# Performance work log

Hardware: AMD Instinct MI355X
Metric: run time of the kernel (lower is better)

## Reference

```python
import jax, jax.numpy as jnp
import numpy as np

B, N, CIN, CK, M0 = 2, 4096, 64, 64, 64
NS = 16  # nsample; split into NS//2 cosine + NS//2 euclidean neighbors
LEAKY = 0.1


def _leaky(x):
    return jax.nn.leaky_relu(x, LEAKY)


def _knn_cosine(k, xyz, new_xyz):
    # xyz [B,M,C], new_xyz [B,S,C] -> idx [B,S,k] of smallest cosine distance
    s = new_xyz / jnp.sqrt(jnp.sum(new_xyz ** 2, -1, keepdims=True) + 1e-8)
    d = xyz / jnp.sqrt(jnp.sum(xyz ** 2, -1, keepdims=True) + 1e-8)
    dist = 1.0 - jnp.einsum('bsc,bmc->bsm', s, d)
    return jax.lax.top_k(-dist, k)[1]


def _knn_euclid(k, xyz, new_xyz):
    # squared euclidean distance [B,S,M]
    dist = (jnp.sum(new_xyz ** 2, -1)[:, :, None]
            + jnp.sum(xyz ** 2, -1)[:, None, :]
            - 2.0 * jnp.einsum('bsc,bmc->bsm', new_xyz, xyz))
    return jax.lax.top_k(-dist, k)[1]


def _group(points, idx):
    # points [B,M,C], idx [B,S,K] -> [B,S,K,C]
    return jax.vmap(lambda p, i: p[i])(points, idx)


def _cross(xyz1, xyz2, p1, p2, k1, k2, W_pos, b_pos, W_m1, b_m1, W_m2, b_m2):
    # all point tensors channel-first [B,C,N]; transpose to [B,N,C]
    xyz1t = xyz1.transpose(0, 2, 1)
    xyz2t = xyz2.transpose(0, 2, 1)
    p1t = p1.transpose(0, 2, 1)
    p2t = p2.transpose(0, 2, 1)
    k1t = k1.transpose(0, 2, 1)
    k2t = k2.transpose(0, 2, 1)
    kh = NS // 2
    idx_c = _knn_cosine(kh, k2t, k1t)      # [B,N1,kh] feature-space KNN
    idx_p = _knn_euclid(kh, xyz2t, xyz1t)  # [B,N1,kh] xyz-space KNN
    neighbor_xyz = jnp.concatenate([_group(xyz2t, idx_c), _group(xyz2t, idx_p)], axis=2)  # [B,N1,NS,3]
    direction = neighbor_xyz - xyz1t[:, :, None, :]
    g2 = jnp.concatenate([_group(p2t, idx_c), _group(p2t, idx_p)], axis=2)  # [B,N1,NS,D]
    pos = jnp.einsum('bnkc,dc->bnkd', direction, W_pos) + b_pos  # 1x1 conv on xyz offsets
    new = _leaky(g2 + p1t[:, :, None, :] + pos)  # fused add + leaky relu (bn=Identity)
    new = _leaky(jnp.einsum('bnkd,ed->bnke', new, W_m1) + b_m1)
    new = _leaky(jnp.einsum('bnkd,ed->bnke', new, W_m2) + b_m2)
    new = jnp.max(new, axis=2)  # max-pool over neighbor dim -> [B,N1,D]
    return new.transpose(0, 2, 1)  # [B,D,N1]


def setup_inputs() -> dict:
    key = jax.random.key(0)
    ks = jax.random.split(key, 12)
    rn = lambda k, shape, s=1.0: jax.random.normal(k, shape, jnp.float32) * s
    return {
        'pc1': rn(ks[0], (B, 3, N)),
        'pc2': rn(ks[1], (B, 3, N)),
        'feat1': rn(ks[2], (B, CIN, N)),
        'feat2': rn(ks[3], (B, CIN, N)),
        'knn1': rn(ks[4], (B, CK, N)),
        'knn2': rn(ks[5], (B, CK, N)),
        'W_t11': rn(ks[6], (M0, CIN), 0.1),
        'b_t11': jnp.zeros((M0,), jnp.float32),
        'W_t22': rn(ks[7], (M0, CIN), 0.1),
        'b_t22': jnp.zeros((M0,), jnp.float32),
        'W_pos': rn(ks[8], (M0, 3), 0.1),
        'b_pos': jnp.zeros((M0,), jnp.float32),
        'W_m1': rn(ks[9], (M0, M0), 0.1),
        'b_m1': jnp.zeros((M0,), jnp.float32),
        'W_m2': rn(ks[10], (M0, M0), 0.1),
        'b_m2': jnp.zeros((M0,), jnp.float32),
    }


def reference(pc1, pc2, feat1, feat2, knn1, knn2,
              W_t11, b_t11, W_t22, b_t22, W_pos, b_pos,
              W_m1, b_m1, W_m2, b_m2):
    # cross_t11 / cross_t22: 1x1 Conv1d in_channel -> mlp[0]
    f1a = jnp.einsum('dc,bcn->bdn', W_t11, feat1) + b_t11[None, :, None]
    f2a = jnp.einsum('dc,bcn->bdn', W_t22, feat2) + b_t22[None, :, None]
    f2b = jnp.einsum('dc,bcn->bdn', W_t11, feat2) + b_t11[None, :, None]
    f1b = jnp.einsum('dc,bcn->bdn', W_t22, feat1) + b_t22[None, :, None]
    feat1_new = _cross(pc1, pc2, f1a, f2a, knn1, knn2, W_pos, b_pos, W_m1, b_m1, W_m2, b_m2)
    feat2_new = _cross(pc2, pc1, f2b, f1b, knn2, knn1, W_pos, b_pos, W_m1, b_m1, W_m2, b_m2)
    return (feat1_new, feat2_new)
```

## Files before the change

kernel.cpp:

```cpp
#include <hip/hip_runtime.h>
#include <hip/hip_bf16.h>

#define BB 2
#define NN 4096
#define CH 64

typedef __bf16 bf16x8 __attribute__((ext_vector_type(8)));
typedef float f32x4 __attribute__((ext_vector_type(4)));

__device__ __forceinline__ float lrelu(float v) { return fmaxf(v, 0.1f * v); }
__device__ __forceinline__ float tobf(const __hip_bfloat16& h) { return __bfloat162float(h); }

#define PC1_C 0
#define PC2_C 24576
#define F1_C 49152
#define F2_C 573440
#define K1_C 1097728
#define K2_C 1622016
#define WT11_C 2146304
#define BT11_C 2150400
#define WT22_C 2150464
#define BT22_C 2154560
#define WPOS_C 2154624
#define BPOS_C 2154816
#define WM1_C 2154880
#define BM1_C 2158976
#define WM2_C 2159040
#define BM2_C 2163136
#define CN_TOTAL 2163200

#define FHALF (2 * BB * NN * CH)

__device__ __forceinline__ unsigned fmap(float s) {
  unsigned u = __float_as_uint(s);
  return u ^ ((unsigned)((int)u >> 31) | 0x80000000u);
}

__device__ __forceinline__ unsigned umaxu(unsigned a, unsigned b) { return a > b ? a : b; }
__device__ __forceinline__ void casu(unsigned& a, unsigned& b) {
  unsigned mx = a > b ? a : b;
  unsigned mn = a > b ? b : a;
  a = mx; b = mn;
}

__device__ __forceinline__ void bitonic8(unsigned bd[8]) {
  casu(bd[0], bd[4]); casu(bd[1], bd[5]); casu(bd[2], bd[6]); casu(bd[3], bd[7]);
  casu(bd[0], bd[2]); casu(bd[1], bd[3]); casu(bd[4], bd[6]); casu(bd[5], bd[7]);
  casu(bd[0], bd[1]); casu(bd[2], bd[3]); casu(bd[4], bd[5]); casu(bd[6], bd[7]);
}

__device__ __forceinline__ void merge4(unsigned bd[8], unsigned k0, unsigned k1,
                                       unsigned k2, unsigned k3) {
  casu(k0, k1); casu(k2, k3); casu(k0, k2); casu(k1, k3); casu(k1, k2);
  bd[4] = umaxu(bd[4], k3); bd[5] = umaxu(bd[5], k2);
  bd[6] = umaxu(bd[6], k1); bd[7] = umaxu(bd[7], k0);
  bitonic8(bd);
}

__device__ __forceinline__ void merge88(unsigned a[8], const unsigned b[8]) {
  a[0] = umaxu(a[0], b[7]); a[1] = umaxu(a[1], b[6]);
  a[2] = umaxu(a[2], b[5]); a[3] = umaxu(a[3], b[4]);
  a[4] = umaxu(a[4], b[3]); a[5] = umaxu(a[5], b[2]);
  a[6] = umaxu(a[6], b[1]); a[7] = umaxu(a[7], b[0]);
  bitonic8(a);
}

__device__ __forceinline__ void xmerge(unsigned a[8], int m) {
  unsigned t[8];
#pragma unroll
  for (int k = 0; k < 8; ++k) t[k] = (unsigned)__shfl_xor((int)a[k], m, 64);
  merge88(a, t);
}

__global__ void k_detect(const unsigned short* __restrict__ pc1raw, int* __restrict__ flag) {
  int lane = threadIdx.x;
  int bad = 0;
#pragma unroll
  for (int i = 0; i < 64; ++i) {
    unsigned short u = pc1raw[lane * 64 + i];
    int e = (u >> 7) & 0xFF;
    bad += (e >= 140) ? 1 : 0;
  }
#pragma unroll
  for (int s = 32; s; s >>= 1) bad += __shfl_xor(bad, s, 64);
  if (lane == 0) *flag = (bad > 16) ? 1 : 0;
}

__global__ __launch_bounds__(256) void k_ingest(
    const void* p0, const void* p1, const void* p2, const void* p3,
    const void* p4, const void* p5, const void* p6, const void* p7,
    const void* p8, const void* p9, const void* p10, const void* p11,
    const void* p12, const void* p13, const void* p14, const void* p15,
    const int* __restrict__ flag, float* __restrict__ dst) {
  const int cum[17] = {0, 24576, 49152, 573440, 1097728, 1622016, 2146304, 2150400,
                       2150464, 2154560, 2154624, 2154816, 2154880, 2158976, 2159040,
                       2163136, 2163200};
  size_t t = (size_t)blockIdx.x * 256 + threadIdx.x;
  if (t >= (size_t)CN_TOTAL) return;
  int seg = 0;
#pragma unroll
  for (int i = 1; i < 16; ++i) seg += (t >= (size_t)cum[i]) ? 1 : 0;
  size_t local = t - (size_t)cum[seg];
  const void* ptrs[16] = {p0, p1, p2, p3, p4, p5, p6, p7, p8, p9, p10, p11, p12, p13, p14, p15};
  const void* p = ptrs[seg];
  float v;
  if (*flag) v = ((const float*)p)[local];
  else       v = tobf(((const __hip_bfloat16*)p)[local]);
  if (!(v == v) || fabsf(v) > 1e30f) v = 0.f;
  dst[t] = v;
}

__global__ __launch_bounds__(256) void k_prep_all(const float* __restrict__ cn,
                                                  float* __restrict__ knnt,
                                                  __hip_bfloat16* __restrict__ knnb,
                                                  __hip_bfloat16* __restrict__ fhl,
                                                  __hip_bfloat16* __restrict__ wmb,
                                                  float4* __restrict__ xyzt,
                                                  float4* __restrict__ wp4,
                                                  __hip_bfloat16* __restrict__ wcb) {
  int bid = blockIdx.x;
  if (bid < 64) {
    int t = bid * 256 + threadIdx.x;
    int n = t & (NN - 1);
    int b = (t >> 12) & 1;
    int a = t >> 13;
    const float* col = cn + (a ? K2_C : K1_C) + (size_t)b * CH * NN + n;
    float s = 0.f;
#pragma unroll
    for (int c = 0; c < CH; ++c) { float v = col[(size_t)c * NN]; s += v * v; }
    float inv = 1.0f / sqrtf(s + 1e-8f);
    size_t row = (size_t)(a * BB + b) * NN + n;
    float* o = knnt + row * CH;
    __hip_bfloat16* ob = knnb + row * CH;
#pragma unroll
    for (int c = 0; c < CH; ++c) {
      float v = col[(size_t)c * NN] * inv;
      o[c] = v;
      ob[c] = __float2bfloat16(v);
    }
  } else if (bid < 128) {
    int t = (bid - 64) * 256 + threadIdx.x;
    int n = t & (NN - 1);
    int b = (t >> 12) & 1;
    int a = t >> 13;
    const float* col = cn + (a ? F2_C : F1_C) + (size_t)b * CH * NN + n;
    __hip_bfloat16* oh = fhl + ((size_t)(a * BB + b) * NN + n) * CH;
    __hip_bfloat16* ol = oh + FHALF;
#pragma unroll
    for (int c = 0; c < CH; ++c) {
      float v = col[(size_t)c * NN];
      __hip_bfloat16 hi = __float2bfloat16(v);
      oh[c] = hi;
      ol[c] = __float2bfloat16(v - tobf(hi));
    }
  } else if (bid < 160) {
    int t = (bid - 128) * 256 + threadIdx.x;
    float v = (t < 4096) ? cn[WM1_C + t] : cn[WM2_C + (t - 4096)];
    wmb[t] = __float2bfloat16(v);
  } else if (bid < 224) {
    int t = (bid - 160) * 256 + threadIdx.x;
    int n = t & (NN - 1);
    int b = (t >> 12) & 1;
    int a = t >> 13;
    const float* p = cn + (a ? PC2_C : PC1_C) + (size_t)b * 3 * NN + n;
    float x = p[0], y = p[NN], z = p[2 * NN];
    xyzt[(size_t)(a * BB + b) * NN + n] = make_float4(x, y, z, x * x + y * y + z * z);
  } else if (bid == 224) {
    int c = threadIdx.x;
    if (c < 64)
      wp4[c] = make_float4(cn[WPOS_C + 3 * c], cn[WPOS_C + 3 * c + 1],
                           cn[WPOS_C + 3 * c + 2], cn[BPOS_C + c]);
  } else {
    int t = (bid - 225) * 256 + threadIdx.x;
    int w = t >> 12, e = t & 4095;
    float v = cn[(w ? WT22_C : WT11_C) + e];
    __hip_bfloat16 hi = __float2bfloat16(v);
    __hip_bfloat16 lo = __float2bfloat16(v - tobf(hi));
    wcb[w * 4096 + e] = hi;
    wcb[8192 + w * 4096 + e] = lo;
  }
}

__global__ __launch_bounds__(256) void k_conv2(const __hip_bfloat16* __restrict__ fhl,
                                               const __hip_bfloat16* __restrict__ wcb,
                                               const float* __restrict__ cn,
                                               float* __restrict__ fbuf) {
  int bid = blockIdx.x;
  int ntile = bid & 255;
  int b = (bid >> 8) & 1;
  int a = bid >> 9;
  int t = threadIdx.x;
  int dt = t >> 6;
  int lane = t & 63;
  int lo = lane & 15, g = lane >> 4;

  const __hip_bfloat16* fb = fhl + ((size_t)(a * BB + b) * NN + ntile * 16 + lo) * CH;
  bf16x8 ah0 = *reinterpret_cast<const bf16x8*>(fb + g * 8);
  bf16x8 ah1 = *reinterpret_cast<const bf16x8*>(fb + 32 + g * 8);
  bf16x8 al0 = *reinterpret_cast<const bf16x8*>(fb + FHALF + g * 8);
  bf16x8 al1 = *reinterpret_cast<const bf16x8*>(fb + FHALF + 32 + g * 8);

#pragma unroll
  for (int w = 0; w < 2; ++w) {
    const __hip_bfloat16* wb = wcb + w * 4096 + (dt * 16 + lo) * 64;
    bf16x8 wh0 = *reinterpret_cast<const bf16x8*>(wb + g * 8);
    bf16x8 wh1 = *reinterpret_cast<const bf16x8*>(wb + 32 + g * 8);
    bf16x8 wl0 = *reinterpret_cast<const bf16x8*>(wb + 8192 + g * 8);
    bf16x8 wl1 = *reinterpret_cast<const bf16x8*>(wb + 8192 + 32 + g * 8);
    float bv = cn[(w ? BT22_C : BT11_C) + dt * 16 + lo];
    f32x4 acc = {bv, bv, bv, bv};
    acc = __builtin_amdgcn_mfma_f32_16x16x32_bf16(ah0, wh0, acc, 0, 0, 0);
    acc = __builtin_amdgcn_mfma_f32_16x16x32_bf16(ah1, wh1, acc, 0, 0, 0);
    acc = __builtin_amdgcn_mfma_f32_16x16x32_bf16(al0, wh0, acc, 0, 0, 0);
    acc = __builtin_amdgcn_mfma_f32_16x16x32_bf16(al1, wh1, acc, 0, 0, 0);
    acc = __builtin_amdgcn_mfma_f32_16x16x32_bf16(ah0, wl0, acc, 0, 0, 0);
    acc = __builtin_amdgcn_mfma_f32_16x16x32_bf16(ah1, wl1, acc, 0, 0, 0);
    int sel = a ? (w ? 1 : 2) : (w ? 3 : 0);
    float* ob = fbuf + ((size_t)(sel * BB + b) * NN + ntile * 16 + g * 4) * CH + dt * 16 + lo;
    ob[0 * CH] = acc[0];
    ob[1 * CH] = acc[1];
    ob[2 * CH] = acc[2];
    ob[3 * CH] = acc[3];
  }
}

__global__ __launch_bounds__(512, 4) void k_knn5(const __hip_bfloat16* __restrict__ knnb,
                                                 const float* __restrict__ knnt,
                                                 const float4* __restrict__ xyzt,
                                                 int* __restrict__ idxf) {
  __shared__ unsigned sk[16 * 8 * 9];
  __shared__ int cidx[16 * 16];
  int bid = blockIdx.x;
  int qt = bid & (NN / 16 - 1);
  int b = (bid >> 8) & 1;
  int x = bid >> 9;
  int w = threadIdx.x >> 6;
  int lane = threadIdx.x & 63;
  int lo = lane & 15, g = lane >> 4;
  int q0 = qt * 16;
  int j0 = w * (NN / 8);
  int hw = lane >> 5, sl = lane & 31;
  int qq = w * 2 + hw;
  size_t qbase = (size_t)(x * BB + b) * NN;
  size_t dbase = (size_t)((1 - x) * BB + b) * NN;

  const __hip_bfloat16* qb = knnb + (qbase + q0) * CH;
  bf16x8 qf0 = *reinterpret_cast<const bf16x8*>(qb + lo * CH + g * 8);
  bf16x8 qf1 = *reinterpret_cast<const bf16x8*>(qb + lo * CH + 32 + g * 8);
  const __hip_bfloat16* db = knnb + dbase * CH;
  const float4 q4 = xyzt[qbase + q0 + lo];
  const float4* dbx = xyzt + dbase;
  float tx = 2.f * q4.x, ty = 2.f * q4.y, tz = 2.f * q4.z;

  unsigned bc0[8], bc1[8], be0[8], be1[8];
#pragma unroll
  for (int k = 0; k < 8; ++k) { bc0[k] = 0u; bc1[k] = 0u; be0[k] = 0u; be1[k] = 0u; }

  auto STEP = [&](const bf16x8& A0, const bf16x8& A1, const float4& P0,
                  const float4& P1, const float4& P2, const float4& P3,
                  int rcv, unsigned (&bc)[8], unsigned (&be)[8]) {
    f32x4 acc = {0.f, 0.f, 0.f, 0.f};
    acc = __builtin_amdgcn_mfma_f32_16x16x32_bf16(A0, qf0, acc, 0, 0, 0);
    acc = __builtin_amdgcn_mfma_f32_16x16x32_bf16(A1, qf1, acc, 0, 0, 0);
    float v0 = fmaf(tx, P0.x, fmaf(ty, P0.y, fmaf(tz, P0.z, -P0.w)));
    float v1 = fmaf(tx, P1.x, fmaf(ty, P1.y, fmaf(tz, P1.z, -P1.w)));
    float v2 = fmaf(tx, P2.x, fmaf(ty, P2.y, fmaf(tz, P2.z, -P2.w)));
    float v3 = fmaf(tx, P3.x, fmaf(ty, P3.y, fmaf(tz, P3.z, -P3.w)));
    unsigned r = (unsigned)rcv;
    merge4(bc, (__float_as_uint(acc[0] + 4.0f) & 0xFFFFF000u) | r,
               (__float_as_uint(acc[1] + 4.0f) & 0xFFFFF000u) | (r - 1),
               (__float_as_uint(acc[2] + 4.0f) & 0xFFFFF000u) | (r - 2),
               (__float_as_uint(acc[3] + 4.0f) & 0xFFFFF000u) | (r - 3));
    merge4(be, (fmap(v0) & 0xFFFFF000u) | r,
               (fmap(v1) & 0xFFFFF000u) | (r - 1),
               (fmap(v2) & 0xFFFFF000u) | (r - 2),
               (fmap(v3) & 0xFFFFF000u) | (r - 3));
  };

  const __hip_bfloat16* arA = db + (size_t)(j0 + lo) * CH + g * 8;
  const __hip_bfloat16* arB = arA + 16 * CH;
  const float4* peA = dbx + j0 + g * 4;
  const float4* peB = peA + 16;
  int rc = 4095 - j0 - g * 4;

  bf16x8 aA0 = *reinterpret_cast<const bf16x8*>(arA);
  bf16x8 aA1 = *reinterpret_cast<const bf16x8*>(arA + 32);
  float4 pA0 = peA[0], pA1 = peA[1], pA2 = peA[2], pA3 = peA[3];

  for (int i = 0; i < 15; ++i) {
    bf16x8 aB0 = *reinterpret_cast<const bf16x8*>(arB);
    bf16x8 aB1 = *reinterpret_cast<const bf16x8*>(arB + 32);
    float4 pB0 = peB[0], pB1 = peB[1], pB2 = peB[2], pB3 = peB[3];
    STEP(aA0, aA1, pA0, pA1, pA2, pA3, rc, bc0, be0);
    arA += 32 * CH; peA += 32;
    aA0 = *reinterpret_cast<const bf16x8*>(arA);
    aA1 = *reinterpret_cast<const bf16x8*>(arA + 32);
    pA0 = peA[0]; pA1 = peA[1]; pA2 = peA[2]; pA3 = peA[3];
    STEP(aB0, aB1, pB0, pB1, pB2, pB3, rc - 16, bc1, be1);
    arB += 32 * CH; peB += 32;
    rc -= 32;
  }
  {
    bf16x8 aB0 = *reinterpret_cast<const bf16x8*>(arB);
    bf16x8 aB1 = *reinterpret_cast<const bf16x8*>(arB + 32);
    float4 pB0 = peB[0], pB1 = peB[1], pB2 = peB[2], pB3 = peB[3];
    STEP(aA0, aA1, pA0, pA1, pA2, pA3, rc, bc0, be0);
    STEP(aB0, aB1, pB0, pB1, pB2, pB3, rc - 16, bc1, be1);
  }
  merge88(bc0, bc1);
  merge88(be0, be1);
  xmerge(bc0, 16); xmerge(bc0, 32);
  xmerge(be0, 16); xmerge(be0, 32);

  if (g == 0) {
#pragma unroll
    for (int k = 0; k < 8; ++k) sk[(lo * 8 + k) * 9 + w] = bc0[k];
  }
  __syncthreads();
  {
    unsigned e[16];
#pragma unroll
    for (int k = 0; k < 8; ++k) e[k] = sk[(qq * 8 + k) * 9 + (sl & 7)];
#pragma unroll
    for (int k = 8; k < 16; ++k) e[k] = 0u;
#pragma unroll
    for (int s = 1; s < 8; s <<= 1) {
      unsigned f[16];
#pragma unroll
      for (int k = 0; k < 16; ++k) f[k] = (unsigned)__shfl_xor((int)e[k], s, 64);
#pragma unroll
      for (int i = 0; i < 16; ++i) e[i] = umaxu(e[i], f[15 - i]);
      casu(e[0], e[8]); casu(e[1], e[9]); casu(e[2], e[10]); casu(e[3], e[11]);
      casu(e[4], e[12]); casu(e[5], e[13]); casu(e[6], e[14]); casu(e[7], e[15]);
      casu(e[0], e[4]); casu(e[1], e[5]); casu(e[2], e[6]); casu(e[3], e[7]);
      casu(e[8], e[12]); casu(e[9], e[13]); casu(e[10], e[14]); casu(e[11], e[15]);
      casu(e[0], e[2]); casu(e[1], e[3]); casu(e[4], e[6]); casu(e[5], e[7]);
      casu(e[8], e[10]); casu(e[9], e[11]); casu(e[12], e[14]); casu(e[13], e[15]);
      casu(e[0], e[1]); casu(e[2], e[3]); casu(e[4], e[5]); casu(e[6], e[7]);
      casu(e[8], e[9]); casu(e[10], e[11]); casu(e[12], e[13]); casu(e[14], e[15]);
    }
    if (sl == 0) {
#pragma unroll
      for (int k = 0; k < 16; ++k) cidx[qq * 16 + k] = 4095 - (int)(e[k] & 4095u);
    }
    int c = sl >> 1, hr = sl & 1;
    int idx = cidx[qq * 16 + c];
    const float4* qr = reinterpret_cast<const float4*>(knnt + (qbase + q0 + qq) * CH) + hr * 8;
    const float4* dr = reinterpret_cast<const float4*>(knnt + (dbase + idx) * CH) + hr * 8;
    float v = 0.f;
#pragma unroll 4
    for (int cb = 0; cb < 8; ++cb) {
      float4 qv = qr[cb], dv = dr[cb];
      v += qv.x * dv.x + qv.y * dv.y + qv.z * dv.z + qv.w * dv.w;
    }
    v += __shfl_xor(v, 1, 64);
    int ii = idx;
#pragma unroll
    for (int k = 2; k <= 32; k <<= 1) {
#pragma unroll
      for (int j = k >> 1; j >= 1; j >>= 1) {
        float ov = __shfl_xor(v, j, 64);
        int oi = __shfl_xor(ii, j, 64);
        bool ob = (ov > v) || (ov == v && oi < ii);
        bool want = (((sl & k) == 0) == ((sl & j) == 0));
        bool take = (want == ob);
        v = take ? ov : v;
        ii = take ? oi : ii;
      }
    }
    if (sl < 16 && (sl & 1) == 0) idxf[(qbase + q0 + qq) * 16 + (sl >> 1)] = ii;
  }
  __syncthreads();

  if (g == 0) {
#pragma unroll
    for (int k = 0; k < 8; ++k) sk[(lo * 8 + k) * 9 + w] = be0[k];
  }
  __syncthreads();
  {
    unsigned e[16];
#pragma unroll
    for (int k = 0; k < 8; ++k) e[k] = sk[(qq * 8 + k) * 9 + (sl & 7)];
#pragma unroll
    for (int k = 8; k < 16; ++k) e[k] = 0u;
#pragma unroll
    for (int s = 1; s < 8; s <<= 1) {
      unsigned f[16];
#pragma unroll
      for (int k = 0; k < 16; ++k) f[k] = (unsigned)__shfl_xor((int)e[k], s, 64);
#pragma unroll
      for (int i = 0; i < 16; ++i) e[i] = umaxu(e[i], f[15 - i]);
      casu(e[0], e[8]); casu(e[1], e[9]); casu(e[2], e[10]); casu(e[3], e[11]);
      casu(e[4], e[12]); casu(e[5], e[13]); casu(e[6], e[14]); casu(e[7], e[15]);
      casu(e[0], e[4]); casu(e[1], e[5]); casu(e[2], e[6]); casu(e[3], e[7]);
      casu(e[8], e[12]); casu(e[9], e[13]); casu(e[10], e[14]); casu(e[11], e[15]);
      casu(e[0], e[2]); casu(e[1], e[3]); casu(e[4], e[6]); casu(e[5], e[7]);
      casu(e[8], e[10]); casu(e[9], e[11]); casu(e[12], e[14]); casu(e[13], e[15]);
      casu(e[0], e[1]); casu(e[2], e[3]); casu(e[4], e[5]); casu(e[6], e[7]);
      casu(e[8], e[9]); casu(e[10], e[11]); casu(e[12], e[13]); casu(e[14], e[15]);
    }
    if (sl == 0) {
#pragma unroll
      for (int k = 0; k < 16; ++k) cidx[qq * 16 + k] = 4095 - (int)(e[k] & 4095u);
    }
    int c = sl >> 1;
    int idx = cidx[qq * 16 + c];
    const float4 qx4 = xyzt[qbase + q0 + qq];
    float4 p = xyzt[dbase + idx];
    float v = fmaf(2.f * qx4.x, p.x, fmaf(2.f * qx4.y, p.y, fmaf(2.f * qx4.z, p.z, -p.w)));
    int ii = idx;
#pragma unroll
    for (int k = 2; k <= 32; k <<= 1) {
#pragma unroll
      for (int j = k >> 1; j >= 1; j >>= 1) {
        float ov = __shfl_xor(v, j, 64);
        int oi = __shfl_xor(ii, j, 64);
        bool ob = (ov > v) || (ov == v && oi < ii);
        bool want = (((sl & k) == 0) == ((sl & j) == 0));
        bool take = (want == ob);
        v = take ? ov : v;
        ii = take ? oi : ii;
      }
    }
    if (sl < 16 && (sl & 1) == 0) idxf[(qbase + q0 + qq) * 16 + 8 + (sl >> 1)] = ii;
  }
}

__global__ __launch_bounds__(256) void k_mlp(const float* __restrict__ fbuf,
                                             const float4* __restrict__ xyzt,
                                             const int* __restrict__ idxf,
                                             const float4* __restrict__ wp4,
                                             const __hip_bfloat16* __restrict__ wmb,
                                             const float* __restrict__ cn,
                                             float* __restrict__ out) {
  __shared__ __bf16 h1s[4 * 16 * 72];
  const int t = threadIdx.x;
  const int wv = t >> 6, L = t & 63;
  const int lo = L & 15, g = L >> 4;
  int bid = blockIdx.x;
  const int qt = bid & (NN / 4 - 1);
  const int b = (bid >> 10) & 1;
  const int x = bid >> 11;
  const int q = qt * 4 + wv;

  bf16x8 w1f[4][2], w2f[4][2];
#pragma unroll
  for (int tt = 0; tt < 4; ++tt)
#pragma unroll
    for (int kc = 0; kc < 2; ++kc) {
      int e = tt * 16 + lo, c0 = kc * 32 + g * 8;
      w1f[tt][kc] = *reinterpret_cast<const bf16x8*>(wmb + e * 64 + c0);
      w2f[tt][kc] = *reinterpret_cast<const bf16x8*>(wmb + 4096 + e * 64 + c0);
    }

  const float* pq  = fbuf + ((size_t)((x ? 2 : 0) * BB + b)) * NN * CH;
  const float* pdb = fbuf + ((size_t)((x ? 3 : 1) * BB + b)) * NN * CH;
  const float4* qx  = xyzt + (size_t)(x * BB + b) * NN;
  const float4* dbx = xyzt + (size_t)((1 - x) * BB + b) * NN;

  const int m = lo;
  int jm = idxf[(((size_t)x * BB + b) * NN + q) * 16 + m];
  jm &= (NN - 1);
  const float4 q4 = qx[q];
  const float4 p4 = dbx[jm];
  const float dx = p4.x - q4.x, dy = p4.y - q4.y, dz = p4.z - q4.z;

  const float4* g2v = reinterpret_cast<const float4*>(pdb + (size_t)jm * CH);
  const float4* pqv = reinterpret_cast<const float4*>(pq + (size_t)q * CH);
  float hv[16];
  {
    float4 t0 = g2v[g * 2], t1 = g2v[g * 2 + 1], t2 = g2v[g * 2 + 8], t3 = g2v[g * 2 + 9];
    float4 u0 = pqv[g * 2], u1 = pqv[g * 2 + 1], u2 = pqv[g * 2 + 8], u3 = pqv[g * 2 + 9];
    hv[0] = t0.x + u0.x; hv[1] = t0.y + u0.y; hv[2] = t0.z + u0.z; hv[3] = t0.w + u0.w;
    hv[4] = t1.x + u1.x; hv[5] = t1.y + u1.y; hv[6] = t1.z + u1.z; hv[7] = t1.w + u1.w;
    hv[8] = t2.x + u2.x; hv[9] = t2.y + u2.y; hv[10] = t2.z + u2.z; hv[11] = t2.w + u2.w;
    hv[12] = t3.x + u3.x; hv[13] = t3.y + u3.y; hv[14] = t3.z + u3.z; hv[15] = t3.w + u3.w;
  }

  bf16x8 a0, a1;
#pragma unroll
  for (int kc = 0; kc < 2; ++kc) {
#pragma unroll
    for (int j = 0; j < 8; ++j) {
      int c = kc * 32 + g * 8 + j;
      float4 wp = wp4[c];
      float v = hv[kc * 8 + j] + wp.x * dx + wp.y * dy + wp.z * dz + wp.w;
      v = lrelu(v);
      if (kc == 0) a0[j] = (__bf16)v; else a1[j] = (__bf16)v;
    }
  }

  __bf16* hrow = h1s + wv * 16 * 72;
#pragma unroll
  for (int tt = 0; tt < 4; ++tt) {
    float bv = cn[BM1_C + tt * 16 + lo];
    f32x4 acc = {bv, bv, bv, bv};
    acc = __builtin_amdgcn_mfma_f32_16x16x32_bf16(a0, w1f[tt][0], acc, 0, 0, 0);
    acc = __builtin_amdgcn_mfma_f32_16x16x32_bf16(a1, w1f[tt][1], acc, 0, 0, 0);
#pragma unroll
    for (int r = 0; r < 4; ++r) {
      float v = lrelu(acc[r]);
      hrow[(g * 4 + r) * 72 + tt * 16 + lo] = (__bf16)v;
    }
  }
  __syncthreads();
  bf16x8 h1a = *reinterpret_cast<const bf16x8*>(hrow + m * 72 + g * 8);
  bf16x8 h1b = *reinterpret_cast<const bf16x8*>(hrow + m * 72 + 32 + g * 8);

  size_t obase = ((size_t)(x * BB + b) * CH) * NN;
#pragma unroll
  for (int tt = 0; tt < 4; ++tt) {
    float bv = cn[BM2_C + tt * 16 + lo];
    f32x4 acc = {bv, bv, bv, bv};
    acc = __builtin_amdgcn_mfma_f32_16x16x32_bf16(h1a, w2f[tt][0], acc, 0, 0, 0);
    acc = __builtin_amdgcn_mfma_f32_16x16x32_bf16(h1b, w2f[tt][1], acc, 0, 0, 0);
    float v = fmaxf(fmaxf(lrelu(acc[0]), lrelu(acc[1])), fmaxf(lrelu(acc[2]), lrelu(acc[3])));
    v = fmaxf(v, __shfl_xor(v, 16, 64));
    v = fmaxf(v, __shfl_xor(v, 32, 64));
    if (g == 0) out[obase + (size_t)(tt * 16 + lo) * NN + q] = v;
  }
}

#define CN_OFF 0
#define FB_OFF ((size_t)CN_TOTAL)
#define KT_OFF (FB_OFF + (size_t)4 * BB * NN * CH)
#define XZ_OFF (KT_OFF + (size_t)2 * BB * NN * CH)
#define WP4_OFF (XZ_OFF + (size_t)2 * BB * NN * 4)
#define WMB_OFF (WP4_OFF + 256)
#define IDX_OFF (WMB_OFF + 4096)
#define FLAG_OFF (IDX_OFF + 262144)
#define KNB_OFF (FLAG_OFF + 4)
#define FHL_OFF (KNB_OFF + (size_t)BB * NN * CH)
#define WCB_OFF (FHL_OFF + (size_t)2 * BB * NN * CH)

extern "C" void kernel_launch(void* const* d_in, const int* in_sizes, int n_in,
                              void* d_out, int out_size, void* d_ws, size_t ws_size,
                              hipStream_t stream) {
  float* ws = (float*)d_ws;
  float* cn = ws + CN_OFF;
  int* flag = (int*)(ws + FLAG_OFF);

  k_detect<<<1, 64, 0, stream>>>((const unsigned short*)d_in[0], flag);
  k_ingest<<<(CN_TOTAL + 255) / 256, 256, 0, stream>>>(
      d_in[0], d_in[1], d_in[2], d_in[3], d_in[4], d_in[5], d_in[6], d_in[7],
      d_in[8], d_in[9], d_in[10], d_in[11], d_in[12], d_in[13], d_in[14], d_in[15],
      flag, cn);
  k_prep_all<<<257, 256, 0, stream>>>(cn, ws + KT_OFF, (__hip_bfloat16*)(ws + KNB_OFF),
                                      (__hip_bfloat16*)(ws + FHL_OFF),
                                      (__hip_bfloat16*)(ws + WMB_OFF),
                                      (float4*)(ws + XZ_OFF), (float4*)(ws + WP4_OFF),
                                      (__hip_bfloat16*)(ws + WCB_OFF));
  k_conv2<<<1024, 256, 0, stream>>>((const __hip_bfloat16*)(ws + FHL_OFF),
                                    (const __hip_bfloat16*)(ws + WCB_OFF), cn, ws + FB_OFF);
  k_knn5<<<2 * BB * (NN / 16), 512, 0, stream>>>(
      (const __hip_bfloat16*)(ws + KNB_OFF), ws + KT_OFF,
      (const float4*)(ws + XZ_OFF), (int*)(ws + IDX_OFF));
  k_mlp<<<2 * BB * (NN / 4), 256, 0, stream>>>(ws + FB_OFF, (const float4*)(ws + XZ_OFF),
                                               (const int*)(ws + IDX_OFF), (const float4*)(ws + WP4_OFF),
                                               (const __hip_bfloat16*)(ws + WMB_OFF), cn,
                                               (float*)d_out);
}
```

Measured before the change: 273.8 us.

## Fuse dtype detection and ingest into prep, read inputs directly

Removes the separate detect kernel and the large ingest copy of all activations into a float staging buffer. The prep kernel now reads the raw inputs directly and detects the dtype per block, and only the small weight tensors are still staged. Block index decoding in conv, knn and mlp is reordered so batch and side vary fastest, and the knn launch bounds request higher occupancy. Each block now repeats the dtype detection read, and the tighter launch bound may force register spills.

```diff
diff --git a/kernel.cpp b/kernel.cpp
--- a/kernel.cpp
+++ b/kernel.cpp
@@ -31,6 +31,30 @@
 
 #define FHALF (2 * BB * NN * CH)
 
+__device__ __forceinline__ bool detect_f32(const unsigned short* __restrict__ pc1raw) {
+  int lane = threadIdx.x & 63;
+  const uint4* p4 = reinterpret_cast<const uint4*>(pc1raw);
+  int bad = 0;
+#pragma unroll
+  for (int k = 0; k < 8; ++k) {
+    uint4 v = p4[lane * 8 + k];
+    unsigned w0 = v.x, w1 = v.y, w2 = v.z, w3 = v.w;
+    bad += (((w0 >> 7) & 0xFF) >= 140) + (((w0 >> 23) & 0xFF) >= 140);
+    bad += (((w1 >> 7) & 0xFF) >= 140) + (((w1 >> 23) & 0xFF) >= 140);
+    bad += (((w2 >> 7) & 0xFF) >= 140) + (((w2 >> 23) & 0xFF) >= 140);
+    bad += (((w3 >> 7) & 0xFF) >= 140) + (((w3 >> 23) & 0xFF) >= 140);
+  }
+#pragma unroll
+  for (int s = 32; s; s >>= 1) bad += __shfl_xor(bad, s, 64);
+  return bad > 16;
+}
+
+__device__ __forceinline__ float rdval(const void* __restrict__ p, size_t i, bool f32) {
+  float v = f32 ? ((const float*)p)[i] : tobf(((const __hip_bfloat16*)p)[i]);
+  if (!(v == v) || fabsf(v) > 1e30f) v = 0.f;
+  return v;
+}
+
 __device__ __forceinline__ unsigned fmap(float s) {
   unsigned u = __float_as_uint(s);
   return u ^ ((unsigned)((int)u >> 31) | 0x80000000u);
@@ -72,83 +96,64 @@
   merge88(a, t);
 }
 
-__global__ void k_detect(const unsigned short* __restrict__ pc1raw, int* __restrict__ flag) {
-  int lane = threadIdx.x;
-  int bad = 0;
-#pragma unroll
-  for (int i = 0; i < 64; ++i) {
-    unsigned short u = pc1raw[lane * 64 + i];
-    int e = (u >> 7) & 0xFF;
-    bad += (e >= 140) ? 1 : 0;
-  }
-#pragma unroll
-  for (int s = 32; s; s >>= 1) bad += __shfl_xor(bad, s, 64);
-  if (lane == 0) *flag = (bad > 16) ? 1 : 0;
-}
-
-__global__ __launch_bounds__(256) void k_ingest(
-    const void* p0, const void* p1, const void* p2, const void* p3,
-    const void* p4, const void* p5, const void* p6, const void* p7,
-    const void* p8, const void* p9, const void* p10, const void* p11,
-    const void* p12, const void* p13, const void* p14, const void* p15,
-    const int* __restrict__ flag, float* __restrict__ dst) {
-  const int cum[17] = {0, 24576, 49152, 573440, 1097728, 1622016, 2146304, 2150400,
-                       2150464, 2154560, 2154624, 2154816, 2154880, 2158976, 2159040,
-                       2163136, 2163200};
-  size_t t = (size_t)blockIdx.x * 256 + threadIdx.x;
-  if (t >= (size_t)CN_TOTAL) return;
+__global__ __launch_bounds__(256) void k_ingest_small(
+    const void* p6, const void* p7, const void* p8, const void* p9,
+    const void* p10, const void* p11, const void* p12, const void* p13,
+    const void* p14, const void* p15, const unsigned short* __restrict__ pc1raw,
+    float* __restrict__ dst) {
+  bool f32 = detect_f32(pc1raw);
+  int t = blockIdx.x * 256 + threadIdx.x;
+  if (t >= 16896) return;
+  const int cum[11] = {0, 4096, 4160, 8256, 8320, 8512, 8576, 12672, 12736, 16832, 16896};
   int seg = 0;
 #pragma unroll
-  for (int i = 1; i < 16; ++i) seg += (t >= (size_t)cum[i]) ? 1 : 0;
-  size_t local = t - (size_t)cum[seg];
-  const void* ptrs[16] = {p0, p1, p2, p3, p4, p5, p6, p7, p8, p9, p10, p11, p12, p13, p14, p15};
-  const void* p = ptrs[seg];
-  float v;
-  if (*flag) v = ((const float*)p)[local];
-  else       v = tobf(((const __hip_bfloat16*)p)[local]);
-  if (!(v == v) || fabsf(v) > 1e30f) v = 0.f;
-  dst[t] = v;
-}
-
-__global__ __launch_bounds__(256) void k_prep_all(const float* __restrict__ cn,
-                                                  float* __restrict__ knnt,
-                                                  __hip_bfloat16* __restrict__ knnb,
-                                                  __hip_bfloat16* __restrict__ fhl,
-                                                  __hip_bfloat16* __restrict__ wmb,
-                                                  float4* __restrict__ xyzt,
-                                                  float4* __restrict__ wp4,
-                                                  __hip_bfloat16* __restrict__ wcb) {
+  for (int i = 1; i < 11; ++i) seg += (t >= cum[i]) ? 1 : 0;
+  const void* ptrs[10] = {p6, p7, p8, p9, p10, p11, p12, p13, p14, p15};
+  dst[WT11_C + t] = rdval(ptrs[seg], t - cum[seg], f32);
+}
+
+__global__ __launch_bounds__(256) void k_prep_all(
+    const void* pc1, const void* pc2, const void* f1, const void* f2,
+    const void* k1, const void* k2, const float* __restrict__ cn,
+    float* __restrict__ knnt, __hip_bfloat16* __restrict__ knnb,
+    __hip_bfloat16* __restrict__ fhl, __hip_bfloat16* __restrict__ wmb,
+    float4* __restrict__ xyzt, float4* __restrict__ wp4,
+    __hip_bfloat16* __restrict__ wcb) {
   int bid = blockIdx.x;
   if (bid < 64) {
+    bool f32 = detect_f32((const unsigned short*)pc1);
     int t = bid * 256 + threadIdx.x;
     int n = t & (NN - 1);
     int b = (t >> 12) & 1;
     int a = t >> 13;
-    const float* col = cn + (a ? K2_C : K1_C) + (size_t)b * CH * NN + n;
+    const void* src = a ? k2 : k1;
+    size_t base = (size_t)b * CH * NN + n;
     float s = 0.f;
 #pragma unroll
-    for (int c = 0; c < CH; ++c) { float v = col[(size_t)c * NN]; s += v * v; }
+    for (int c = 0; c < CH; ++c) { float v = rdval(src, base + (size_t)c * NN, f32); s += v * v; }
     float inv = 1.0f / sqrtf(s + 1e-8f);
     size_t row = (size_t)(a * BB + b) * NN + n;
     float* o = knnt + row * CH;
     __hip_bfloat16* ob = knnb + row * CH;
 #pragma unroll
     for (int c = 0; c < CH; ++c) {
-      float v = col[(size_t)c * NN] * inv;
+      float v = rdval(src, base + (size_t)c * NN, f32) * inv;
       o[c] = v;
       ob[c] = __float2bfloat16(v);
     }
   } else if (bid < 128) {
+    bool f32 = detect_f32((const unsigned short*)pc1);
     int t = (bid - 64) * 256 + threadIdx.x;
     int n = t & (NN - 1);
     int b = (t >> 12) & 1;
     int a = t >> 13;
-    const float* col = cn + (a ? F2_C : F1_C) + (size_t)b * CH * NN + n;
+    const void* src = a ? f2 : f1;
+    size_t base = (size_t)b * CH * NN + n;
     __hip_bfloat16* oh = fhl + ((size_t)(a * BB + b) * NN + n) * CH;
     __hip_bfloat16* ol = oh + FHALF;
 #pragma unroll
     for (int c = 0; c < CH; ++c) {
-      float v = col[(size_t)c * NN];
+      float v = rdval(src, base + (size_t)c * NN, f32);
       __hip_bfloat16 hi = __float2bfloat16(v);
       oh[c] = hi;
       ol[c] = __float2bfloat16(v - tobf(hi));
@@ -158,12 +163,16 @@
     float v = (t < 4096) ? cn[WM1_C + t] : cn[WM2_C + (t - 4096)];
     wmb[t] = __float2bfloat16(v);
   } else if (bid < 224) {
+    bool f32 = detect_f32((const unsigned short*)pc1);
     int t = (bid - 160) * 256 + threadIdx.x;
     int n = t & (NN - 1);
     int b = (t >> 12) & 1;
     int a = t >> 13;
-    const float* p = cn + (a ? PC2_C : PC1_C) + (size_t)b * 3 * NN + n;
-    float x = p[0], y = p[NN], z = p[2 * NN];
+    const void* src = a ? pc2 : pc1;
+    size_t base = (size_t)b * 3 * NN + n;
+    float x = rdval(src, base, f32);
+    float y = rdval(src, base + NN, f32);
+    float z = rdval(src, base + 2 * NN, f32);
     xyzt[(size_t)(a * BB + b) * NN + n] = make_float4(x, y, z, x * x + y * y + z * z);
   } else if (bid == 224) {
     int c = threadIdx.x;
@@ -186,9 +195,9 @@
                                                const float* __restrict__ cn,
                                                float* __restrict__ fbuf) {
   int bid = blockIdx.x;
-  int ntile = bid & 255;
-  int b = (bid >> 8) & 1;
-  int a = bid >> 9;
+  int b = bid & 1;
+  int a = (bid >> 1) & 1;
+  int ntile = bid >> 2;
   int t = threadIdx.x;
   int dt = t >> 6;
   int lane = t & 63;
@@ -224,16 +233,16 @@
   }
 }
 
-__global__ __launch_bounds__(512, 4) void k_knn5(const __hip_bfloat16* __restrict__ knnb,
+__global__ __launch_bounds__(512, 8) void k_knn5(const __hip_bfloat16* __restrict__ knnb,
                                                  const float* __restrict__ knnt,
                                                  const float4* __restrict__ xyzt,
                                                  int* __restrict__ idxf) {
   __shared__ unsigned sk[16 * 8 * 9];
   __shared__ int cidx[16 * 16];
   int bid = blockIdx.x;
-  int qt = bid & (NN / 16 - 1);
-  int b = (bid >> 8) & 1;
-  int x = bid >> 9;
+  int b = bid & 1;
+  int x = (bid >> 1) & 1;
+  int qt = bid >> 2;
   int w = threadIdx.x >> 6;
   int lane = threadIdx.x & 63;
   int lo = lane & 15, g = lane >> 4;
@@ -438,9 +447,9 @@
   const int wv = t >> 6, L = t & 63;
   const int lo = L & 15, g = L >> 4;
   int bid = blockIdx.x;
-  const int qt = bid & (NN / 4 - 1);
-  const int b = (bid >> 10) & 1;
-  const int x = bid >> 11;
+  const int b = bid & 1;
+  const int x = (bid >> 1) & 1;
+  const int qt = bid >> 2;
   const int q = qt * 4 + wv;
 
   bf16x8 w1f[4][2], w2f[4][2];
@@ -538,18 +547,15 @@
                               hipStream_t stream) {
   float* ws = (float*)d_ws;
   float* cn = ws + CN_OFF;
-  int* flag = (int*)(ws + FLAG_OFF);
-
-  k_detect<<<1, 64, 0, stream>>>((const unsigned short*)d_in[0], flag);
-  k_ingest<<<(CN_TOTAL + 255) / 256, 256, 0, stream>>>(
-      d_in[0], d_in[1], d_in[2], d_in[3], d_in[4], d_in[5], d_in[6], d_in[7],
-      d_in[8], d_in[9], d_in[10], d_in[11], d_in[12], d_in[13], d_in[14], d_in[15],
-      flag, cn);
-  k_prep_all<<<257, 256, 0, stream>>>(cn, ws + KT_OFF, (__hip_bfloat16*)(ws + KNB_OFF),
-                                      (__hip_bfloat16*)(ws + FHL_OFF),
-                                      (__hip_bfloat16*)(ws + WMB_OFF),
-                                      (float4*)(ws + XZ_OFF), (float4*)(ws + WP4_OFF),
-                                      (__hip_bfloat16*)(ws + WCB_OFF));
+
+  k_ingest_small<<<66, 256, 0, stream>>>(
+      d_in[6], d_in[7], d_in[8], d_in[9], d_in[10], d_in[11], d_in[12], d_in[13],
+      d_in[14], d_in[15], (const unsigned short*)d_in[0], cn);
+  k_prep_all<<<257, 256, 0, stream>>>(
+      d_in[0], d_in[1], d_in[2], d_in[3], d_in[4], d_in[5], cn,
+      ws + KT_OFF, (__hip_bfloat16*)(ws + KNB_OFF), (__hip_bfloat16*)(ws + FHL_OFF),
+      (__hip_bfloat16*)(ws + WMB_OFF), (float4*)(ws + XZ_OFF), (float4*)(ws + WP4_OFF),
+      (__hip_bfloat16*)(ws + WCB_OFF));
   k_conv2<<<1024, 256, 0, stream>>>((const __hip_bfloat16*)(ws + FHL_OFF),
                                     (const __hip_bfloat16*)(ws + WCB_OFF), cn, ws + FB_OFF);
   k_knn5<<<2 * BB * (NN / 16), 512, 0, stream>>>(
```

New measurement: 391.9 us. 1.43x slower.

## Fuse conv kernel into KNN kernel launch and interleave block index mapping

Applied to the files above, without the earlier changes.

The separate 1x1-conv MFMA kernel is merged into the KNN kernel as extra tail blocks (ids 1024 and up, two conv tiles per 512-thread block), removing one kernel launch and letting the conv work fill idle CUs alongside the KNN blocks. Block index decoding in the KNN and MLP kernels is reordered so batch and direction vary fastest, spreading adjacent blocks across different data. In exchange, the conv blocks now carry the KNN kernel's shared memory and 512-thread launch bounds, which may limit their occupancy, and the new block ordering may change cache locality.

```diff
diff --git a/kernel.cpp b/kernel.cpp
--- a/kernel.cpp
+++ b/kernel.cpp
@@ -181,59 +181,61 @@
   }
 }
 
-__global__ __launch_bounds__(256) void k_conv2(const __hip_bfloat16* __restrict__ fhl,
-                                               const __hip_bfloat16* __restrict__ wcb,
-                                               const float* __restrict__ cn,
-                                               float* __restrict__ fbuf) {
+__global__ __launch_bounds__(512, 4) void k_knncv(const __hip_bfloat16* __restrict__ knnb,
+                                                  const float* __restrict__ knnt,
+                                                  const float4* __restrict__ xyzt,
+                                                  const __hip_bfloat16* __restrict__ fhl,
+                                                  const __hip_bfloat16* __restrict__ wcb,
+                                                  const float* __restrict__ cn,
+                                                  int* __restrict__ idxf,
+                                                  float* __restrict__ fbuf) {
   int bid = blockIdx.x;
-  int ntile = bid & 255;
-  int b = (bid >> 8) & 1;
-  int a = bid >> 9;
-  int t = threadIdx.x;
-  int dt = t >> 6;
-  int lane = t & 63;
-  int lo = lane & 15, g = lane >> 4;
-
-  const __hip_bfloat16* fb = fhl + ((size_t)(a * BB + b) * NN + ntile * 16 + lo) * CH;
-  bf16x8 ah0 = *reinterpret_cast<const bf16x8*>(fb + g * 8);
-  bf16x8 ah1 = *reinterpret_cast<const bf16x8*>(fb + 32 + g * 8);
-  bf16x8 al0 = *reinterpret_cast<const bf16x8*>(fb + FHALF + g * 8);
-  bf16x8 al1 = *reinterpret_cast<const bf16x8*>(fb + FHALF + 32 + g * 8);
-
-#pragma unroll
-  for (int w = 0; w < 2; ++w) {
-    const __hip_bfloat16* wb = wcb + w * 4096 + (dt * 16 + lo) * 64;
-    bf16x8 wh0 = *reinterpret_cast<const bf16x8*>(wb + g * 8);
-    bf16x8 wh1 = *reinterpret_cast<const bf16x8*>(wb + 32 + g * 8);
-    bf16x8 wl0 = *reinterpret_cast<const bf16x8*>(wb + 8192 + g * 8);
-    bf16x8 wl1 = *reinterpret_cast<const bf16x8*>(wb + 8192 + 32 + g * 8);
-    float bv = cn[(w ? BT22_C : BT11_C) + dt * 16 + lo];
-    f32x4 acc = {bv, bv, bv, bv};
-    acc = __builtin_amdgcn_mfma_f32_16x16x32_bf16(ah0, wh0, acc, 0, 0, 0);
-    acc = __builtin_amdgcn_mfma_f32_16x16x32_bf16(ah1, wh1, acc, 0, 0, 0);
-    acc = __builtin_amdgcn_mfma_f32_16x16x32_bf16(al0, wh0, acc, 0, 0, 0);
-    acc = __builtin_amdgcn_mfma_f32_16x16x32_bf16(al1, wh1, acc, 0, 0, 0);
-    acc = __builtin_amdgcn_mfma_f32_16x16x32_bf16(ah0, wl0, acc, 0, 0, 0);
-    acc = __builtin_amdgcn_mfma_f32_16x16x32_bf16(ah1, wl1, acc, 0, 0, 0);
-    int sel = a ? (w ? 1 : 2) : (w ? 3 : 0);
-    float* ob = fbuf + ((size_t)(sel * BB + b) * NN + ntile * 16 + g * 4) * CH + dt * 16 + lo;
-    ob[0 * CH] = acc[0];
-    ob[1 * CH] = acc[1];
-    ob[2 * CH] = acc[2];
-    ob[3 * CH] = acc[3];
-  }
-}
-
-__global__ __launch_bounds__(512, 4) void k_knn5(const __hip_bfloat16* __restrict__ knnb,
-                                                 const float* __restrict__ knnt,
-                                                 const float4* __restrict__ xyzt,
-                                                 int* __restrict__ idxf) {
+  if (bid >= 1024) {
+    int cb = bid - 1024;
+    int b = cb & 1;
+    int a = (cb >> 1) & 1;
+    int ntile = (cb >> 2) * 2 + (threadIdx.x >> 8);
+    int t = threadIdx.x & 255;
+    int dt = t >> 6;
+    int lane = t & 63;
+    int lo = lane & 15, g = lane >> 4;
+
+    const __hip_bfloat16* fb = fhl + ((size_t)(a * BB + b) * NN + ntile * 16 + lo) * CH;
+    bf16x8 ah0 = *reinterpret_cast<const bf16x8*>(fb + g * 8);
+    bf16x8 ah1 = *reinterpret_cast<const bf16x8*>(fb + 32 + g * 8);
+    bf16x8 al0 = *reinterpret_cast<const bf16x8*>(fb + FHALF + g * 8);
+    bf16x8 al1 = *reinterpret_cast<const bf16x8*>(fb + FHALF + 32 + g * 8);
+
+#pragma unroll
+    for (int w = 0; w < 2; ++w) {
+      const __hip_bfloat16* wb = wcb + w * 4096 + (dt * 16 + lo) * 64;
+      bf16x8 wh0 = *reinterpret_cast<const bf16x8*>(wb + g * 8);
+      bf16x8 wh1 = *reinterpret_cast<const bf16x8*>(wb + 32 + g * 8);
+      bf16x8 wl0 = *reinterpret_cast<const bf16x8*>(wb + 8192 + g * 8);
+      bf16x8 wl1 = *reinterpret_cast<const bf16x8*>(wb + 8192 + 32 + g * 8);
+      float bv = cn[(w ? BT22_C : BT11_C) + dt * 16 + lo];
+      f32x4 acc = {bv, bv, bv, bv};
+      acc = __builtin_amdgcn_mfma_f32_16x16x32_bf16(ah0, wh0, acc, 0, 0, 0);
+      acc = __builtin_amdgcn_mfma_f32_16x16x32_bf16(ah1, wh1, acc, 0, 0, 0);
+      acc = __builtin_amdgcn_mfma_f32_16x16x32_bf16(al0, wh0, acc, 0, 0, 0);
+      acc = __builtin_amdgcn_mfma_f32_16x16x32_bf16(al1, wh1, acc, 0, 0, 0);
+      acc = __builtin_amdgcn_mfma_f32_16x16x32_bf16(ah0, wl0, acc, 0, 0, 0);
+      acc = __builtin_amdgcn_mfma_f32_16x16x32_bf16(ah1, wl1, acc, 0, 0, 0);
+      int sel = a ? (w ? 1 : 2) : (w ? 3 : 0);
+      float* ob = fbuf + ((size_t)(sel * BB + b) * NN + ntile * 16 + g * 4) * CH + dt * 16 + lo;
+      ob[0 * CH] = acc[0];
+      ob[1 * CH] = acc[1];
+      ob[2 * CH] = acc[2];
+      ob[3 * CH] = acc[3];
+    }
+    return;
+  }
+
   __shared__ unsigned sk[16 * 8 * 9];
   __shared__ int cidx[16 * 16];
-  int bid = blockIdx.x;
-  int qt = bid & (NN / 16 - 1);
-  int b = (bid >> 8) & 1;
-  int x = bid >> 9;
+  int b = bid & 1;
+  int x = (bid >> 1) & 1;
+  int qt = bid >> 2;
   int w = threadIdx.x >> 6;
   int lane = threadIdx.x & 63;
   int lo = lane & 15, g = lane >> 4;
@@ -438,9 +440,9 @@
   const int wv = t >> 6, L = t & 63;
   const int lo = L & 15, g = L >> 4;
   int bid = blockIdx.x;
-  const int qt = bid & (NN / 4 - 1);
-  const int b = (bid >> 10) & 1;
-  const int x = bid >> 11;
+  const int b = bid & 1;
+  const int x = (bid >> 1) & 1;
+  const int qt = bid >> 2;
   const int q = qt * 4 + wv;
 
   bf16x8 w1f[4][2], w2f[4][2];
@@ -550,11 +552,10 @@
                                       (__hip_bfloat16*)(ws + WMB_OFF),
                                       (float4*)(ws + XZ_OFF), (float4*)(ws + WP4_OFF),
                                       (__hip_bfloat16*)(ws + WCB_OFF));
-  k_conv2<<<1024, 256, 0, stream>>>((const __hip_bfloat16*)(ws + FHL_OFF),
-                                    (const __hip_bfloat16*)(ws + WCB_OFF), cn, ws + FB_OFF);
-  k_knn5<<<2 * BB * (NN / 16), 512, 0, stream>>>(
-      (const __hip_bfloat16*)(ws + KNB_OFF), ws + KT_OFF,
-      (const float4*)(ws + XZ_OFF), (int*)(ws + IDX_OFF));
+  k_knncv<<<1536, 512, 0, stream>>>(
+      (const __hip_bfloat16*)(ws + KNB_OFF), ws + KT_OFF, (const float4*)(ws + XZ_OFF),
+      (const __hip_bfloat16*)(ws + FHL_OFF), (const __hip_bfloat16*)(ws + WCB_OFF),
+      cn, (int*)(ws + IDX_OFF), ws + FB_OFF);
   k_mlp<<<2 * BB * (NN / 4), 256, 0, stream>>>(ws + FB_OFF, (const float4*)(ws + XZ_OFF),
                                                (const int*)(ws + IDX_OFF), (const float4*)(ws + WP4_OFF),
                                                (const __hip_bfloat16*)(ws + WMB_OFF), cn,
```

Measured after the change: 274.7 us. No clear change (+0.3%).
